# Performance work log

Hardware: AMD Instinct MI355X
Metric: run time of the kernel (lower is better)

## Reference

```python
import jax, jax.numpy as jnp
import numpy as np

EPS = 1e-5

def setup_inputs() -> dict:
    key = jax.random.key(0)
    ks = jax.random.split(key, 12)
    N, d0, d1, d2, qh, qo = 8192, 128, 256, 256, 128, 1
    state = jax.random.normal(ks[0], (N, d0), dtype=jnp.float32)
    adjacent_matrix = jax.random.uniform(ks[1], (N, N), dtype=jnp.float32)
    s = 0.05
    return {
        "state": state,
        "adjacent_matrix": adjacent_matrix,
        "gamma": jnp.ones((d0,), jnp.float32),
        "beta": jnp.zeros((d0,), jnp.float32),
        "W1": jax.random.normal(ks[2], (d0, d1), jnp.float32) * s,
        "b1": jnp.zeros((d1,), jnp.float32),
        "W2": jax.random.normal(ks[3], (d1, d2), jnp.float32) * s,
        "b2": jnp.zeros((d2,), jnp.float32),
        "Wq1": jax.random.normal(ks[4], (d2, qh), jnp.float32) * s,
        "bq1": jnp.zeros((qh,), jnp.float32),
        "Wq2": jax.random.normal(ks[5], (qh, qo), jnp.float32) * s,
        "bq2": jnp.zeros((qo,), jnp.float32),
    }


def reference(state, adjacent_matrix, gamma, beta, W1, b1, W2, b2, Wq1, bq1, Wq2, bq2):
    # LinkBatchNorm: BatchNorm1d over node (batch) axis, training-mode statistics
    mean = jnp.mean(state, axis=0)
    var = jnp.var(state, axis=0)
    x = (state - mean) * jax.lax.rsqrt(var + EPS) * gamma + beta  # [N, d0]
    # GraphCNN: two layers of relu(A @ X @ W + b)
    h = jax.nn.relu(adjacent_matrix @ (x @ W1) + b1)   # [N, d1]
    h = jax.nn.relu(adjacent_matrix @ (h @ W2) + b2)   # [N, d2]
    # QNetwork: per-node MLP -> Q value
    q = jax.nn.relu(h @ Wq1 + bq1) @ Wq2 + bq2         # [N, 1]
    return q
```

## Files before the change

### kernel.cpp

```cpp
#include <hip/hip_runtime.h>
#include <stdint.h>

#define NN 8192
#define D0 128
#define D1 256
#define D2 256
#define QH 128
#define EPSV 1e-5f

using bf16x8 = __attribute__((ext_vector_type(8))) __bf16;
using f32x4  = __attribute__((ext_vector_type(4))) float;

__device__ __forceinline__ unsigned short f2bf(float f) {
    union { float f; unsigned int u; } v; v.f = f;
    unsigned int r = v.u + 0x7FFFu + ((v.u >> 16) & 1u);
    return (unsigned short)(r >> 16);
}
__device__ __forceinline__ float bf2f(unsigned short h) {
    union { unsigned int u; float f; } v; v.u = ((unsigned int)h) << 16;
    return v.f;
}
__device__ __forceinline__ void async_ld16(const void* g, void* l) {
    __builtin_amdgcn_global_load_lds(
        (__attribute__((address_space(1))) void*)(g),
        (__attribute__((address_space(3))) void*)(l), 16, 0, 0);
}

__global__ void k_zero(float* __restrict__ p) {
    p[blockIdx.x * 256 + threadIdx.x] = 0.f;
}

__global__ void k_stats(const float* __restrict__ state,
                        float* __restrict__ psum, float* __restrict__ psq) {
    int j = threadIdx.x;
    int b = blockIdx.x;
    const float* p = state + (size_t)b * 32 * D0 + j;
    float s = 0.f, sq = 0.f;
#pragma unroll 4
    for (int r = 0; r < 32; ++r) { float x = p[(size_t)r * D0]; s += x; sq += x * x; }
    psum[b * D0 + j] = s;
    psq [b * D0 + j] = sq;
}

__global__ void k_finalize(const float* __restrict__ psum, const float* __restrict__ psq,
                           const float* __restrict__ gamma, const float* __restrict__ beta,
                           const float* __restrict__ W1,
                           float* __restrict__ scale, float* __restrict__ shift,
                           float* __restrict__ c1) {
    __shared__ float s_shift[D0];
    int t = threadIdx.x;
    if (t < D0) {
        float s = 0.f, sq = 0.f;
        for (int b = 0; b < 256; ++b) { s += psum[b * D0 + t]; sq += psq[b * D0 + t]; }
        float mean = s * (1.0f / NN);
        float var  = sq * (1.0f / NN) - mean * mean;
        float sc = gamma[t] * rsqrtf(var + EPSV);
        float sh = beta[t] - mean * sc;
        scale[t] = sc; shift[t] = sh; s_shift[t] = sh;
    }
    __syncthreads();
    float acc = 0.f;
    for (int k = 0; k < D0; ++k) acc += s_shift[k] * W1[(size_t)k * D1 + t];
    c1[t] = acc;
}

__global__ void k_prep_weights(const float* __restrict__ W1, const float* __restrict__ W2,
                               const float* __restrict__ scale,
                               unsigned short* __restrict__ W1st,
                               unsigned short* __restrict__ W2t) {
    int idx = blockIdx.x * 256 + threadIdx.x;
    if (idx < 32768) {
        int n = idx >> 7, k = idx & 127;
        W1st[idx] = f2bf(W1[(size_t)k * D1 + n] * scale[k]);
    } else {
        int i = idx - 32768; int n = i >> 8, k = i & 255;
        W2t[i] = f2bf(W2[(size_t)k * D2 + n]);
    }
}

template <int N, int K, bool A_FP32, bool BIAS>
__global__ __launch_bounds__(256, 4) void k_small_gemm(
        const void* __restrict__ Aptr, const unsigned short* __restrict__ Bt,
        const float* __restrict__ bias, unsigned short* __restrict__ out) {
    constexpr int WN = N / 4;
    constexpr int NJ = WN / 16;
    constexpr int BI = N / 64;
    __shared__ unsigned short Alds[32 * 32];
    __shared__ unsigned short Blds[N * 32];
    int t = threadIdx.x, lane = t & 63, w = t >> 6;
    int m0 = blockIdx.x * 32;
    int lr = lane & 15, lk = (lane >> 4) * 8;
    int wc = w * WN;
    f32x4 acc[2][NJ] = {};

    for (int kk = 0; kk < K; kk += 32) {
        __syncthreads();
        if constexpr (A_FP32) {
            const float* A = (const float*)Aptr;
            int row = t >> 3, kc = (t & 7) * 4;
            float4 v = *(const float4*)(A + (size_t)(m0 + row) * K + kk + kc);
            uint2 p;
            p.x = ((unsigned)f2bf(v.y) << 16) | f2bf(v.x);
            p.y = ((unsigned)f2bf(v.w) << 16) | f2bf(v.z);
            *(uint2*)&Alds[row * 32 + kc] = p;
        } else {
            if (w < 2) {
                const unsigned short* A = (const unsigned short*)Aptr;
                int row = w * 16 + (lane >> 2);
                async_ld16(A + (size_t)(m0 + row) * K + kk + (lane & 3) * 8, &Alds[w * 512]);
            }
        }
#pragma unroll
        for (int i = 0; i < BI; ++i) {
            int n = w * WN + i * 16 + (lane >> 2);
            async_ld16(Bt + (size_t)n * K + kk + (lane & 3) * 8, &Blds[(w * WN + i * 16) * 32]);
        }
        __syncthreads();
        bf16x8 a[2], b[NJ];
#pragma unroll
        for (int i = 0; i < 2; ++i) a[i] = *(const bf16x8*)&Alds[(i * 16 + lr) * 32 + lk];
#pragma unroll
        for (int j = 0; j < NJ; ++j) b[j] = *(const bf16x8*)&Blds[(wc + j * 16 + lr) * 32 + lk];
#pragma unroll
        for (int i = 0; i < 2; ++i)
#pragma unroll
            for (int j = 0; j < NJ; ++j)
                acc[i][j] = __builtin_amdgcn_mfma_f32_16x16x32_bf16(a[i], b[j], acc[i][j], 0, 0, 0);
    }
    int q = lane >> 4;
#pragma unroll
    for (int j = 0; j < NJ; ++j) {
        int n = wc + j * 16 + lr;
        float bv = 0.f;
        if constexpr (BIAS) bv = bias[n];
#pragma unroll
        for (int i = 0; i < 2; ++i) {
#pragma unroll
            for (int r = 0; r < 4; ++r) {
                int m = m0 + i * 16 + q * 4 + r;
                out[(size_t)m * N + n] = f2bf(acc[i][j][r] + bv);
            }
        }
    }
}

__global__ void k_transpose(const unsigned short* __restrict__ in, unsigned short* __restrict__ out,
                            float* __restrict__ colsum) {
    __shared__ unsigned short tile[64 * 68];
    __shared__ float cp[4][64];
    int t = threadIdx.x;
    int r0 = blockIdx.x * 64, c0 = blockIdx.y * 64;
#pragma unroll
    for (int p = 0; p < 4; ++p) {
        int row = (t >> 4) + p * 16, col = (t & 15) * 4;
        *(ushort4*)&tile[row * 68 + col] = *(const ushort4*)&in[(size_t)(r0 + row) * 256 + c0 + col];
    }
    __syncthreads();
    int n = t >> 2;
#pragma unroll
    for (int s = 0; s < 2; ++s) {
        int mo = (t & 3) * 16 + s * 8;
        unsigned short v[8];
#pragma unroll
        for (int e = 0; e < 8; ++e) v[e] = tile[(mo + e) * 68 + n];
        *(uint4*)&out[(size_t)(c0 + n) * NN + r0 + mo] = *(const uint4*)v;
    }
    int col = t & 63, gg = t >> 6;
    float s = 0.f;
#pragma unroll
    for (int r = 0; r < 16; ++r) s += bf2f(tile[(gg * 16 + r) * 68 + col]);
    cp[gg][col] = s;
    __syncthreads();
    if (t < 64) atomicAdd(colsum + c0 + t, cp[0][t] + cp[1][t] + cp[2][t] + cp[3][t]);
}

__global__ __launch_bounds__(512, 2) void k_big_gemm(
        const float* __restrict__ A, const unsigned short* __restrict__ Yt,
        float* __restrict__ Cp, float* __restrict__ rsPart) {
    __shared__ unsigned short Alds[128 * 32];
    __shared__ unsigned short Blds[256 * 32];
    int t = threadIdx.x, lane = t & 63, w = t >> 6;
    int m0 = blockIdx.x * 128;
    int kbeg = blockIdx.y * 2048;
    int wr = (w & 1) * 64, wc = (w >> 1) * 64;
    int lr = lane & 15, lk = (lane >> 4) * 8;
    f32x4 acc[4][4] = {};

    int arow = t >> 3;
    int akc = (t & 7) * 4;
    const float* ag = A + (size_t)(m0 + arow) * NN + kbeg + akc;
    int bn = w * 32 + (lane >> 2);
    const unsigned short* bg = Yt + (size_t)bn * NN + kbeg + (lane & 3) * 8;
    float rs0 = 0.f, rs1 = 0.f;

    for (int kk = 0; kk < 2048; kk += 32) {
        __syncthreads();
        {
            float4 v0 = *(const float4*)(ag + kk);
            float4 v1 = *(const float4*)(ag + (size_t)64 * NN + kk);
            rs0 += v0.x + v0.y + v0.z + v0.w;
            rs1 += v1.x + v1.y + v1.z + v1.w;
            uint2 p0, p1;
            p0.x = ((unsigned)f2bf(v0.y) << 16) | f2bf(v0.x);
            p0.y = ((unsigned)f2bf(v0.w) << 16) | f2bf(v0.z);
            p1.x = ((unsigned)f2bf(v1.y) << 16) | f2bf(v1.x);
            p1.y = ((unsigned)f2bf(v1.w) << 16) | f2bf(v1.z);
            *(uint2*)&Alds[arow * 32 + akc] = p0;
            *(uint2*)&Alds[(arow + 64) * 32 + akc] = p1;
        }
        async_ld16(bg + kk, &Blds[(w * 32) * 32]);
        async_ld16(bg + (size_t)16 * NN + kk, &Blds[(w * 32 + 16) * 32]);
        __syncthreads();
        bf16x8 a[4], b[4];
#pragma unroll
        for (int i = 0; i < 4; ++i) a[i] = *(const bf16x8*)&Alds[(wr + i * 16 + lr) * 32 + lk];
#pragma unroll
        for (int j = 0; j < 4; ++j) b[j] = *(const bf16x8*)&Blds[(wc + j * 16 + lr) * 32 + lk];
#pragma unroll
        for (int i = 0; i < 4; ++i)
#pragma unroll
            for (int j = 0; j < 4; ++j)
                acc[i][j] = __builtin_amdgcn_mfma_f32_16x16x32_bf16(a[i], b[j], acc[i][j], 0, 0, 0);
    }
#pragma unroll
    for (int m = 1; m < 8; m <<= 1) {
        rs0 += __shfl_xor(rs0, m, 64);
        rs1 += __shfl_xor(rs1, m, 64);
    }
    if ((lane & 7) == 0) {
        rsPart[(size_t)blockIdx.y * NN + m0 + arow] = rs0;
        rsPart[(size_t)blockIdx.y * NN + m0 + arow + 64] = rs1;
    }
    float* outp = Cp + (size_t)blockIdx.y * NN * 256;
    int q = lane >> 4;
#pragma unroll
    for (int i = 0; i < 4; ++i)
#pragma unroll
        for (int j = 0; j < 4; ++j) {
            int n = wc + j * 16 + lr;
#pragma unroll
            for (int r = 0; r < 4; ++r) {
                int m = m0 + wr + i * 16 + q * 4 + r;
                outp[(size_t)m * 256 + n] = acc[i][j][r];
            }
        }
}

__global__ void k_s2(const float* __restrict__ colB, const float* __restrict__ colH1,
                     const float* __restrict__ W2, float* __restrict__ s2) {
    int n = threadIdx.x;
    float acc = 0.f;
    for (int k = 0; k < 256; ++k) acc += colH1[k] * W2[(size_t)k * 256 + n];
    s2[n] = colB[n] - acc;
}

template <bool STORE_BF16>
__global__ __launch_bounds__(256) void k_reduce(
        const float* __restrict__ Cp, const float* __restrict__ rsPart,
        const float* __restrict__ bias, const float* __restrict__ sn,
        void* __restrict__ outv, float* __restrict__ colH1) {
    __shared__ float rs_s[32];
    __shared__ float cs[4][256];
    int t = threadIdx.x;
    int m0 = blockIdx.x * 32;
    const size_t S = (size_t)NN * 256;
    if (t < 32) {
        float r = 0.f;
        for (int s = 0; s < 4; ++s) r += rsPart[(size_t)s * NN + m0 + t];
        rs_s[t] = r * (1.0f / 8192.0f);
    }
    __syncthreads();
    int g = t >> 6, cq = (t & 63) * 4;
    float4 snv = *(const float4*)(sn + cq);
    float4 bv  = *(const float4*)(bias + cq);
    float c0 = 0.f, c1a = 0.f, c2 = 0.f, c3 = 0.f;
#pragma unroll
    for (int r8 = 0; r8 < 8; ++r8) {
        int row = m0 + g * 8 + r8;
        size_t base = (size_t)row * 256 + cq;
        float4 a0 = *(const float4*)(Cp + base);
        float4 a1 = *(const float4*)(Cp + S + base);
        float4 a2 = *(const float4*)(Cp + 2 * S + base);
        float4 a3 = *(const float4*)(Cp + 3 * S + base);
        float rsv = rs_s[g * 8 + r8];
        float x0 = fmaxf(a0.x + a1.x + a2.x + a3.x + bv.x - rsv * snv.x, 0.f);
        float x1 = fmaxf(a0.y + a1.y + a2.y + a3.y + bv.y - rsv * snv.y, 0.f);
        float x2 = fmaxf(a0.z + a1.z + a2.z + a3.z + bv.z - rsv * snv.z, 0.f);
        float x3 = fmaxf(a0.w + a1.w + a2.w + a3.w + bv.w - rsv * snv.w, 0.f);
        if constexpr (STORE_BF16) {
            ushort4 o; o.x = f2bf(x0); o.y = f2bf(x1); o.z = f2bf(x2); o.w = f2bf(x3);
            *(ushort4*)((unsigned short*)outv + base) = o;
            c0 += x0; c1a += x1; c2 += x2; c3 += x3;
        } else {
            float4 o; o.x = x0; o.y = x1; o.z = x2; o.w = x3;
            *(float4*)((float*)outv + base) = o;
        }
    }
    if constexpr (STORE_BF16) {
        cs[g][cq] = c0; cs[g][cq + 1] = c1a; cs[g][cq + 2] = c2; cs[g][cq + 3] = c3;
        __syncthreads();
        float tot = cs[0][t] + cs[1][t] + cs[2][t] + cs[3][t];
        atomicAdd(colH1 + t, tot);
    }
}

__global__ __launch_bounds__(128) void k_qhead(
        const float* __restrict__ H2, const float* __restrict__ Wq1,
        const float* __restrict__ bq1, const float* __restrict__ Wq2,
        const float* __restrict__ bq2, float* __restrict__ out) {
    __shared__ float sh[8][256];
    __shared__ float red[2][8];
    int t = threadIdx.x;
    int m0 = blockIdx.x * 8;
#pragma unroll
    for (int i = 0; i < 4; ++i) {
        int idx = i * 512 + t * 4;
        int row = idx >> 8, col = idx & 255;
        *(float4*)&sh[row][col] = *(const float4*)(H2 + (size_t)(m0 + row) * 256 + col);
    }
    __syncthreads();
    float acc[8];
    float bq = bq1[t];
#pragma unroll
    for (int r = 0; r < 8; ++r) acc[r] = bq;
    for (int n = 0; n < 256; ++n) {
        float wv = Wq1[(size_t)n * QH + t];
#pragma unroll
        for (int r = 0; r < 8; ++r) acc[r] = fmaf(sh[r][n], wv, acc[r]);
    }
    float wq2 = Wq2[t];
    float bq2v = bq2[0];
    int lane = t & 63, wv2 = t >> 6;
#pragma unroll
    for (int r = 0; r < 8; ++r) {
        float v = fmaxf(acc[r], 0.f) * wq2;
#pragma unroll
        for (int d = 32; d > 0; d >>= 1) v += __shfl_down(v, d, 64);
        if (lane == 0) red[wv2][r] = v;
    }
    __syncthreads();
    if (t < 8) out[m0 + t] = red[0][t] + red[1][t] + bq2v;
}

extern "C" void kernel_launch(void* const* d_in, const int* in_sizes, int n_in,
                              void* d_out, int out_size, void* d_ws, size_t ws_size,
                              hipStream_t stream) {
    const float* state = (const float*)d_in[0];
    const float* adj   = (const float*)d_in[1];
    const float* gamma = (const float*)d_in[2];
    const float* beta  = (const float*)d_in[3];
    const float* W1    = (const float*)d_in[4];
    const float* b1    = (const float*)d_in[5];
    const float* W2    = (const float*)d_in[6];
    const float* b2    = (const float*)d_in[7];
    const float* Wq1   = (const float*)d_in[8];
    const float* bq1   = (const float*)d_in[9];
    const float* Wq2   = (const float*)d_in[10];
    const float* bq2   = (const float*)d_in[11];
    float* out = (float*)d_out;

    char* ws = (char*)d_ws;
    float* psum  = (float*)(ws + 0);
    float* psq   = (float*)(ws + 131072);
    float* scale = (float*)(ws + 262144);
    float* shift = (float*)(ws + 262656);
    float* c1    = (float*)(ws + 263168);
    float* colA  = (float*)(ws + 264192);
    float* colB  = (float*)(ws + 265216);
    float* colH1 = (float*)(ws + 266240);
    float* s2    = (float*)(ws + 267264);
    unsigned short* W1st = (unsigned short*)(ws + 268288);
    unsigned short* W2t  = (unsigned short*)(ws + 333824);
    unsigned short* Ybuf = (unsigned short*)(ws + (size_t)1  * (1u << 20));
    unsigned short* Ytb  = (unsigned short*)(ws + (size_t)5  * (1u << 20));
    unsigned short* Hbuf = (unsigned short*)(ws + (size_t)9  * (1u << 20));
    float*          H2f  = (float*)(ws + (size_t)13 * (1u << 20));
    float*          rsP  = (float*)(ws + (size_t)21 * (1u << 20));
    float*          Cp   = (float*)(ws + (size_t)22 * (1u << 20));

    k_zero<<<4, 256, 0, stream>>>(colA);
    k_stats<<<256, 128, 0, stream>>>(state, psum, psq);
    k_finalize<<<1, 256, 0, stream>>>(psum, psq, gamma, beta, W1, scale, shift, c1);
    k_prep_weights<<<384, 256, 0, stream>>>(W1, W2, scale, W1st, W2t);

    k_small_gemm<256, 128, true, true><<<256, 256, 0, stream>>>(state, W1st, c1, Ybuf);
    k_transpose<<<dim3(128, 4), 256, 0, stream>>>(Ybuf, Ytb, colA);
    k_big_gemm<<<dim3(64, 4), 512, 0, stream>>>(adj, Ytb, Cp, rsP);
    k_reduce<true><<<256, 256, 0, stream>>>(Cp, rsP, b1, colA, Hbuf, colH1);

    k_small_gemm<256, 256, false, false><<<256, 256, 0, stream>>>(Hbuf, W2t, nullptr, Ybuf);
    k_transpose<<<dim3(128, 4), 256, 0, stream>>>(Ybuf, Ytb, colB);
    k_s2<<<1, 256, 0, stream>>>(colB, colH1, W2, s2);
    k_big_gemm<<<dim3(64, 4), 512, 0, stream>>>(adj, Ytb, Cp, rsP);
    k_reduce<false><<<256, 256, 0, stream>>>(Cp, rsP, b2, s2, H2f, nullptr);

    k_qhead<<<1024, 128, 0, stream>>>(H2f, Wq1, bq1, Wq2, bq2, out);
}
```

Measured before the change: 655.7 us.

## Pre-cast adjacency to bf16 once, async-load A tiles, raise split-K, fuse qhead

A new pass reads the fp32 adjacency matrix once, writes a bf16 copy and computes the row sums. Both big GEMMs then load bf16 A tiles straight into LDS with async loads, using an XOR swizzle, so the fp32 matrix is no longer read and converted twice inside the GEMMs. Split-K goes from 4 to 8 with two more blocks per CU, and the second reduce is fused with the Q-head MLP. This adds a 128MB bf16 workspace plus one extra full pass over A, and doubles the partial-sum traffic in the reduce.

```diff
diff --git a/kernel.cpp b/kernel.cpp
--- a/kernel.cpp
+++ b/kernel.cpp
@@ -24,6 +24,35 @@
     __builtin_amdgcn_global_load_lds(
         (__attribute__((address_space(1))) void*)(g),
         (__attribute__((address_space(3))) void*)(l), 16, 0, 0);
+}
+
+__global__ __launch_bounds__(256) void k_castA(const float* __restrict__ A,
+                                               unsigned short* __restrict__ Abf,
+                                               float* __restrict__ rs) {
+    __shared__ float sred[256];
+    int t = threadIdx.x;
+    size_t row = blockIdx.x;
+    const float* ap = A + row * NN;
+    unsigned short* op = Abf + row * NN;
+    float s = 0.f;
+#pragma unroll
+    for (int i = 0; i < 8; ++i) {
+        int c = i * 1024 + t * 4;
+        float4 v = *(const float4*)(ap + c);
+        s += v.x + v.y + v.z + v.w;
+        ushort4 o; o.x = f2bf(v.x); o.y = f2bf(v.y); o.z = f2bf(v.z); o.w = f2bf(v.w);
+        *(ushort4*)(op + c) = o;
+    }
+    sred[t] = s;
+    __syncthreads();
+    if (t < 128) sred[t] += sred[t + 128];
+    __syncthreads();
+    if (t < 64) {
+        float v = sred[t] + sred[t + 64];
+#pragma unroll
+        for (int d = 32; d > 0; d >>= 1) v += __shfl_down(v, d, 64);
+        if (t == 0) rs[row] = v;
+    }
 }
 
 __global__ void k_zero(float* __restrict__ p) {
@@ -174,65 +203,47 @@
     if (t < 64) atomicAdd(colsum + c0 + t, cp[0][t] + cp[1][t] + cp[2][t] + cp[3][t]);
 }
 
-__global__ __launch_bounds__(512, 2) void k_big_gemm(
-        const float* __restrict__ A, const unsigned short* __restrict__ Yt,
-        float* __restrict__ Cp, float* __restrict__ rsPart) {
+__global__ __launch_bounds__(512, 4) void k_big_gemm2(
+        const unsigned short* __restrict__ Abf, const unsigned short* __restrict__ Yt,
+        float* __restrict__ Cp) {
     __shared__ unsigned short Alds[128 * 32];
     __shared__ unsigned short Blds[256 * 32];
     int t = threadIdx.x, lane = t & 63, w = t >> 6;
     int m0 = blockIdx.x * 128;
-    int kbeg = blockIdx.y * 2048;
+    int kbeg = blockIdx.y * 1024;
     int wr = (w & 1) * 64, wc = (w >> 1) * 64;
-    int lr = lane & 15, lk = (lane >> 4) * 8;
+    int lr = lane & 15, q = lane >> 4;
     f32x4 acc[4][4] = {};
 
-    int arow = t >> 3;
-    int akc = (t & 7) * 4;
-    const float* ag = A + (size_t)(m0 + arow) * NN + kbeg + akc;
-    int bn = w * 32 + (lane >> 2);
-    const unsigned short* bg = Yt + (size_t)bn * NN + kbeg + (lane & 3) * 8;
-    float rs0 = 0.f, rs1 = 0.f;
-
-    for (int kk = 0; kk < 2048; kk += 32) {
+    int srow = lane >> 2;
+    int hsw = (lane & 3) ^ ((srow ^ (srow >> 2)) & 3);
+    const unsigned short* agp = Abf + (size_t)(m0 + w * 16 + srow) * NN + kbeg + hsw * 8;
+    const unsigned short* bg0 = Yt + (size_t)(w * 32 + srow) * NN + kbeg + hsw * 8;
+    const unsigned short* bg1 = Yt + (size_t)(w * 32 + 16 + srow) * NN + kbeg + hsw * 8;
+    unsigned short* aLb = Alds + w * 512;
+    unsigned short* bLb0 = Blds + w * 1024;
+    unsigned short* bLb1 = Blds + w * 1024 + 512;
+    int xsr = (lr ^ (lr >> 2)) & 3;
+    int lks = ((q ^ xsr) & 3) * 8;
+
+    for (int kk = 0; kk < 1024; kk += 32) {
         __syncthreads();
-        {
-            float4 v0 = *(const float4*)(ag + kk);
-            float4 v1 = *(const float4*)(ag + (size_t)64 * NN + kk);
-            rs0 += v0.x + v0.y + v0.z + v0.w;
-            rs1 += v1.x + v1.y + v1.z + v1.w;
-            uint2 p0, p1;
-            p0.x = ((unsigned)f2bf(v0.y) << 16) | f2bf(v0.x);
-            p0.y = ((unsigned)f2bf(v0.w) << 16) | f2bf(v0.z);
-            p1.x = ((unsigned)f2bf(v1.y) << 16) | f2bf(v1.x);
-            p1.y = ((unsigned)f2bf(v1.w) << 16) | f2bf(v1.z);
-            *(uint2*)&Alds[arow * 32 + akc] = p0;
-            *(uint2*)&Alds[(arow + 64) * 32 + akc] = p1;
-        }
-        async_ld16(bg + kk, &Blds[(w * 32) * 32]);
-        async_ld16(bg + (size_t)16 * NN + kk, &Blds[(w * 32 + 16) * 32]);
+        async_ld16(agp + kk, aLb);
+        async_ld16(bg0 + kk, bLb0);
+        async_ld16(bg1 + kk, bLb1);
         __syncthreads();
         bf16x8 a[4], b[4];
 #pragma unroll
-        for (int i = 0; i < 4; ++i) a[i] = *(const bf16x8*)&Alds[(wr + i * 16 + lr) * 32 + lk];
-#pragma unroll
-        for (int j = 0; j < 4; ++j) b[j] = *(const bf16x8*)&Blds[(wc + j * 16 + lr) * 32 + lk];
+        for (int i = 0; i < 4; ++i) a[i] = *(const bf16x8*)&Alds[(wr + i * 16 + lr) * 32 + lks];
+#pragma unroll
+        for (int j = 0; j < 4; ++j) b[j] = *(const bf16x8*)&Blds[(wc + j * 16 + lr) * 32 + lks];
 #pragma unroll
         for (int i = 0; i < 4; ++i)
 #pragma unroll
             for (int j = 0; j < 4; ++j)
                 acc[i][j] = __builtin_amdgcn_mfma_f32_16x16x32_bf16(a[i], b[j], acc[i][j], 0, 0, 0);
     }
-#pragma unroll
-    for (int m = 1; m < 8; m <<= 1) {
-        rs0 += __shfl_xor(rs0, m, 64);
-        rs1 += __shfl_xor(rs1, m, 64);
-    }
-    if ((lane & 7) == 0) {
-        rsPart[(size_t)blockIdx.y * NN + m0 + arow] = rs0;
-        rsPart[(size_t)blockIdx.y * NN + m0 + arow + 64] = rs1;
-    }
     float* outp = Cp + (size_t)blockIdx.y * NN * 256;
-    int q = lane >> 4;
 #pragma unroll
     for (int i = 0; i < 4; ++i)
 #pragma unroll
@@ -254,92 +265,103 @@
     s2[n] = colB[n] - acc;
 }
 
-template <bool STORE_BF16>
-__global__ __launch_bounds__(256) void k_reduce(
-        const float* __restrict__ Cp, const float* __restrict__ rsPart,
+__global__ __launch_bounds__(256) void k_reduce8(
+        const float* __restrict__ Cp, const float* __restrict__ rsA,
         const float* __restrict__ bias, const float* __restrict__ sn,
-        void* __restrict__ outv, float* __restrict__ colH1) {
-    __shared__ float rs_s[32];
+        unsigned short* __restrict__ out, float* __restrict__ colH1) {
+    __shared__ float rs_s[16];
     __shared__ float cs[4][256];
     int t = threadIdx.x;
-    int m0 = blockIdx.x * 32;
+    int m0 = blockIdx.x * 16;
     const size_t S = (size_t)NN * 256;
-    if (t < 32) {
-        float r = 0.f;
-        for (int s = 0; s < 4; ++s) r += rsPart[(size_t)s * NN + m0 + t];
-        rs_s[t] = r * (1.0f / 8192.0f);
-    }
+    if (t < 16) rs_s[t] = rsA[m0 + t] * (1.0f / 8192.0f);
     __syncthreads();
     int g = t >> 6, cq = (t & 63) * 4;
     float4 snv = *(const float4*)(sn + cq);
     float4 bv  = *(const float4*)(bias + cq);
     float c0 = 0.f, c1a = 0.f, c2 = 0.f, c3 = 0.f;
 #pragma unroll
-    for (int r8 = 0; r8 < 8; ++r8) {
-        int row = m0 + g * 8 + r8;
-        size_t base = (size_t)row * 256 + cq;
-        float4 a0 = *(const float4*)(Cp + base);
-        float4 a1 = *(const float4*)(Cp + S + base);
-        float4 a2 = *(const float4*)(Cp + 2 * S + base);
-        float4 a3 = *(const float4*)(Cp + 3 * S + base);
-        float rsv = rs_s[g * 8 + r8];
-        float x0 = fmaxf(a0.x + a1.x + a2.x + a3.x + bv.x - rsv * snv.x, 0.f);
-        float x1 = fmaxf(a0.y + a1.y + a2.y + a3.y + bv.y - rsv * snv.y, 0.f);
-        float x2 = fmaxf(a0.z + a1.z + a2.z + a3.z + bv.z - rsv * snv.z, 0.f);
-        float x3 = fmaxf(a0.w + a1.w + a2.w + a3.w + bv.w - rsv * snv.w, 0.f);
-        if constexpr (STORE_BF16) {
-            ushort4 o; o.x = f2bf(x0); o.y = f2bf(x1); o.z = f2bf(x2); o.w = f2bf(x3);
-            *(ushort4*)((unsigned short*)outv + base) = o;
-            c0 += x0; c1a += x1; c2 += x2; c3 += x3;
-        } else {
-            float4 o; o.x = x0; o.y = x1; o.z = x2; o.w = x3;
-            *(float4*)((float*)outv + base) = o;
-        }
-    }
-    if constexpr (STORE_BF16) {
-        cs[g][cq] = c0; cs[g][cq + 1] = c1a; cs[g][cq + 2] = c2; cs[g][cq + 3] = c3;
-        __syncthreads();
-        float tot = cs[0][t] + cs[1][t] + cs[2][t] + cs[3][t];
-        atomicAdd(colH1 + t, tot);
-    }
-}
-
-__global__ __launch_bounds__(128) void k_qhead(
-        const float* __restrict__ H2, const float* __restrict__ Wq1,
-        const float* __restrict__ bq1, const float* __restrict__ Wq2,
-        const float* __restrict__ bq2, float* __restrict__ out) {
-    __shared__ float sh[8][256];
-    __shared__ float red[2][8];
+    for (int r4 = 0; r4 < 4; ++r4) {
+        int row = g * 4 + r4;
+        size_t base = (size_t)(m0 + row) * 256 + cq;
+        float4 a = {0.f, 0.f, 0.f, 0.f};
+#pragma unroll
+        for (int s = 0; s < 8; ++s) {
+            float4 p = *(const float4*)(Cp + (size_t)s * S + base);
+            a.x += p.x; a.y += p.y; a.z += p.z; a.w += p.w;
+        }
+        float rsv = rs_s[row];
+        float x0 = fmaxf(a.x + bv.x - rsv * snv.x, 0.f);
+        float x1 = fmaxf(a.y + bv.y - rsv * snv.y, 0.f);
+        float x2 = fmaxf(a.z + bv.z - rsv * snv.z, 0.f);
+        float x3 = fmaxf(a.w + bv.w - rsv * snv.w, 0.f);
+        ushort4 o; o.x = f2bf(x0); o.y = f2bf(x1); o.z = f2bf(x2); o.w = f2bf(x3);
+        *(ushort4*)(out + base) = o;
+        c0 += x0; c1a += x1; c2 += x2; c3 += x3;
+    }
+    cs[g][cq] = c0; cs[g][cq + 1] = c1a; cs[g][cq + 2] = c2; cs[g][cq + 3] = c3;
+    __syncthreads();
+    float tot = cs[0][t] + cs[1][t] + cs[2][t] + cs[3][t];
+    atomicAdd(colH1 + t, tot);
+}
+
+__global__ __launch_bounds__(256) void k_reduce_qhead(
+        const float* __restrict__ Cp, const float* __restrict__ rsA,
+        const float* __restrict__ bias, const float* __restrict__ sn,
+        const float* __restrict__ Wq1, const float* __restrict__ bq1,
+        const float* __restrict__ Wq2, const float* __restrict__ bq2,
+        float* __restrict__ out) {
+    __shared__ float sh[16][256];
+    __shared__ float rs_s[16];
+    __shared__ float red[4][8];
     int t = threadIdx.x;
-    int m0 = blockIdx.x * 8;
-#pragma unroll
-    for (int i = 0; i < 4; ++i) {
-        int idx = i * 512 + t * 4;
-        int row = idx >> 8, col = idx & 255;
-        *(float4*)&sh[row][col] = *(const float4*)(H2 + (size_t)(m0 + row) * 256 + col);
-    }
-    __syncthreads();
-    float acc[8];
-    float bq = bq1[t];
-#pragma unroll
-    for (int r = 0; r < 8; ++r) acc[r] = bq;
+    int m0 = blockIdx.x * 16;
+    const size_t S = (size_t)NN * 256;
+    if (t < 16) rs_s[t] = rsA[m0 + t] * (1.0f / 8192.0f);
+    __syncthreads();
+    int g = t >> 6, cq = (t & 63) * 4;
+    float4 snv = *(const float4*)(sn + cq);
+    float4 bv  = *(const float4*)(bias + cq);
+#pragma unroll
+    for (int r4 = 0; r4 < 4; ++r4) {
+        int row = g * 4 + r4;
+        size_t base = (size_t)(m0 + row) * 256 + cq;
+        float4 a = {0.f, 0.f, 0.f, 0.f};
+#pragma unroll
+        for (int s = 0; s < 8; ++s) {
+            float4 p = *(const float4*)(Cp + (size_t)s * S + base);
+            a.x += p.x; a.y += p.y; a.z += p.z; a.w += p.w;
+        }
+        float rsv = rs_s[row];
+        float4 o;
+        o.x = fmaxf(a.x + bv.x - rsv * snv.x, 0.f);
+        o.y = fmaxf(a.y + bv.y - rsv * snv.y, 0.f);
+        o.z = fmaxf(a.z + bv.z - rsv * snv.z, 0.f);
+        o.w = fmaxf(a.w + bv.w - rsv * snv.w, 0.f);
+        *(float4*)&sh[row][cq] = o;
+    }
+    __syncthreads();
+    int h = t & 127, rg = t >> 7;
+    float acc[8] = {};
     for (int n = 0; n < 256; ++n) {
-        float wv = Wq1[(size_t)n * QH + t];
-#pragma unroll
-        for (int r = 0; r < 8; ++r) acc[r] = fmaf(sh[r][n], wv, acc[r]);
-    }
-    float wq2 = Wq2[t];
-    float bq2v = bq2[0];
-    int lane = t & 63, wv2 = t >> 6;
+        float wv = Wq1[(size_t)n * QH + h];
+#pragma unroll
+        for (int r = 0; r < 8; ++r) acc[r] = fmaf(sh[rg * 8 + r][n], wv, acc[r]);
+    }
+    float b1v = bq1[h], w2v = Wq2[h];
+    int wid = t >> 6, lane = t & 63;
 #pragma unroll
     for (int r = 0; r < 8; ++r) {
-        float v = fmaxf(acc[r], 0.f) * wq2;
+        float v = fmaxf(acc[r] + b1v, 0.f) * w2v;
 #pragma unroll
         for (int d = 32; d > 0; d >>= 1) v += __shfl_down(v, d, 64);
-        if (lane == 0) red[wv2][r] = v;
-    }
-    __syncthreads();
-    if (t < 8) out[m0 + t] = red[0][t] + red[1][t] + bq2v;
+        if (lane == 0) red[wid][r] = v;
+    }
+    __syncthreads();
+    if (t < 16) {
+        int rg2 = t >> 3, r = t & 7;
+        out[m0 + rg2 * 8 + r] = red[rg2 * 2][r] + red[rg2 * 2 + 1][r] + bq2[0];
+    }
 }
 
 extern "C" void kernel_launch(void* const* d_in, const int* in_sizes, int n_in,
@@ -374,10 +396,11 @@
     unsigned short* Ybuf = (unsigned short*)(ws + (size_t)1  * (1u << 20));
     unsigned short* Ytb  = (unsigned short*)(ws + (size_t)5  * (1u << 20));
     unsigned short* Hbuf = (unsigned short*)(ws + (size_t)9  * (1u << 20));
-    float*          H2f  = (float*)(ws + (size_t)13 * (1u << 20));
-    float*          rsP  = (float*)(ws + (size_t)21 * (1u << 20));
+    float*          rsA  = (float*)(ws + (size_t)14 * (1u << 20));
     float*          Cp   = (float*)(ws + (size_t)22 * (1u << 20));
-
+    unsigned short* Abf  = (unsigned short*)(ws + (size_t)128 * (1u << 20));
+
+    k_castA<<<8192, 256, 0, stream>>>(adj, Abf, rsA);
     k_zero<<<4, 256, 0, stream>>>(colA);
     k_stats<<<256, 128, 0, stream>>>(state, psum, psq);
     k_finalize<<<1, 256, 0, stream>>>(psum, psq, gamma, beta, W1, scale, shift, c1);
@@ -385,14 +408,12 @@
 
     k_small_gemm<256, 128, true, true><<<256, 256, 0, stream>>>(state, W1st, c1, Ybuf);
     k_transpose<<<dim3(128, 4), 256, 0, stream>>>(Ybuf, Ytb, colA);
-    k_big_gemm<<<dim3(64, 4), 512, 0, stream>>>(adj, Ytb, Cp, rsP);
-    k_reduce<true><<<256, 256, 0, stream>>>(Cp, rsP, b1, colA, Hbuf, colH1);
+    k_big_gemm2<<<dim3(64, 8), 512, 0, stream>>>(Abf, Ytb, Cp);
+    k_reduce8<<<512, 256, 0, stream>>>(Cp, rsA, b1, colA, Hbuf, colH1);
 
     k_small_gemm<256, 256, false, false><<<256, 256, 0, stream>>>(Hbuf, W2t, nullptr, Ybuf);
     k_transpose<<<dim3(128, 4), 256, 0, stream>>>(Ybuf, Ytb, colB);
     k_s2<<<1, 256, 0, stream>>>(colB, colH1, W2, s2);
-    k_big_gemm<<<dim3(64, 4), 512, 0, stream>>>(adj, Ytb, Cp, rsP);
-    k_reduce<false><<<256, 256, 0, stream>>>(Cp, rsP, b2, s2, H2f, nullptr);
-
-    k_qhead<<<1024, 128, 0, stream>>>(H2f, Wq1, bq1, Wq2, bq2, out);
-}
+    k_big_gemm2<<<dim3(64, 8), 512, 0, stream>>>(Abf, Ytb, Cp);
+    k_reduce_qhead<<<512, 256, 0, stream>>>(Cp, rsA, b2, s2, Wq1, bq1, Wq2, bq2, out);
+}
```

Result: faster. 608.1 us (-7.3%).
